# Kernel optimization log

Measured on AMD Instinct MI355X. Metric: run time of the kernel, lower is better.

The kernel has to match this reference:

```python
import jax, jax.numpy as jnp
import numpy as np

N_NODES = 50000
N_EDGES = 600000
IN_CH = 128
HID = 128
OUT_CH = 16
N_REL = 8
NEG_SLOPE = 0.2


def glorot(key, shape):
    fan_in, fan_out = shape[-2], shape[-1]
    lim = (6.0 / (fan_in + fan_out)) ** 0.5
    return jax.random.uniform(key, shape, jnp.float32, -lim, lim)


def setup_inputs() -> dict:
    key = jax.random.key(0)
    ks = jax.random.split(key, 16)
    x = jax.random.normal(ks[0], (N_NODES, IN_CH), jnp.float32)
    edge_index = jax.random.randint(ks[1], (2, N_EDGES), 0, N_NODES, jnp.int64)
    edge_type = jax.random.randint(ks[2], (N_EDGES,), 0, N_REL, jnp.int64)
    return {
        "x": x,
        "W1": glorot(ks[3], (N_REL, IN_CH, HID)),
        "q1": glorot(ks[4], (HID, 1)),
        "k1": glorot(ks[5], (HID, 1)),
        "b1": jnp.zeros((HID,), jnp.float32),
        "W2": glorot(ks[6], (N_REL, HID, HID)),
        "q2": glorot(ks[7], (HID, 1)),
        "k2": glorot(ks[8], (HID, 1)),
        "b2": jnp.zeros((HID,), jnp.float32),
        "lin_w": glorot(ks[9], (HID, OUT_CH)),
        "lin_b": jnp.zeros((OUT_CH,), jnp.float32),
        "edge_index": edge_index,
        "edge_type": edge_type,
    }


def rgat_conv(x, W, q, k, b, src, dst, etype, n_nodes):
    # Per-relation linear transform of all nodes: [R, N, H]
    xw = jnp.einsum('ni,rio->rno', x, W)
    hj = xw[etype, src]  # transformed source features per edge [E, H]
    hi = xw[etype, dst]  # transformed target features per edge [E, H]
    # additive self-attention logits (heads=1, dim=1): [E, 1]
    a = jax.nn.leaky_relu(hi @ q + hj @ k, NEG_SLOPE)
    # segment softmax over incoming edges of each target node (across-relation)
    amax = jax.ops.segment_max(a, dst, num_segments=n_nodes)  # [N, 1]
    e = jnp.exp(a - amax[dst])
    denom = jax.ops.segment_sum(e, dst, num_segments=n_nodes)  # [N, 1]
    alpha = e / denom[dst]
    # weighted scatter-add aggregation + bias
    out = jax.ops.segment_sum(alpha * hj, dst, num_segments=n_nodes)
    return out + b


def reference(x, W1, q1, k1, b1, W2, q2, k2, b2, lin_w, lin_b, edge_index, edge_type):
    src, dst = edge_index[0], edge_index[1]
    n = x.shape[0]
    h = jax.nn.relu(rgat_conv(x, W1, q1, k1, b1, src, dst, edge_type, n))
    h = jax.nn.relu(rgat_conv(h, W2, q2, k2, b2, src, dst, edge_type, n))
    h = h @ lin_w + lin_b                 # [N, out]
    g = jnp.mean(h, axis=0, keepdims=True)  # global_mean_pool -> [1, out]
    return jax.nn.log_softmax(g, axis=-1)
```

## Files before the change

### kernel.cpp

```cpp
#include <hip/hip_runtime.h>

#define CH 128
#define N_REL 8
#define OUT_CH 16
#define NEG_SLOPE 0.2f

typedef short short8 __attribute__((ext_vector_type(8)));
typedef float f32x4 __attribute__((ext_vector_type(4)));

__device__ __forceinline__ unsigned short f2bf(float f) {
    unsigned u = __float_as_uint(f);
    return (unsigned short)((u + 0x7fffu + ((u >> 16) & 1u)) >> 16);
}


__device__ __forceinline__ void dev_cast(const float* __restrict__ X,
                                         unsigned short* __restrict__ Xb,
                                         long total, int b, int tid) {
    long i = ((long)b * 256 + tid) * 8;
    if (i >= total) return;
    float4 v0 = *(const float4*)(X + i);
    float4 v1 = *(const float4*)(X + i + 4);
    ushort4 a, c;
    a.x = f2bf(v0.x); a.y = f2bf(v0.y); a.z = f2bf(v0.z); a.w = f2bf(v0.w);
    c.x = f2bf(v1.x); c.y = f2bf(v1.y); c.z = f2bf(v1.z); c.w = f2bf(v1.w);
    *(ushort4*)(Xb + i) = a;
    *(ushort4*)(Xb + i + 4) = c;
}

__device__ __forceinline__ void dev_wqk(const float* __restrict__ W,
                                        const float* __restrict__ qv,
                                        const float* __restrict__ kv,
                                        float* __restrict__ wq, float* __restrict__ wk,
                                        int rb, int tid) {
    int r = rb * 2 + (tid >> 7);
    int i = tid & 127;
    const float* row = W + ((size_t)r * CH + i) * CH;
    float aq = 0.f, ak = 0.f;
    for (int o = 0; o < CH; ++o) { float w = row[o]; aq += w * qv[o]; ak += w * kv[o]; }
    wq[r * CH + i] = aq;
    wk[r * CH + i] = ak;
}

__device__ __forceinline__ void dev_wpack(const float* __restrict__ W,
                                          unsigned short* __restrict__ Wpk, int t) {
    int lane = t & 63, ks = (t >> 6) & 3, ct = (t >> 8) & 7, r = t >> 11;
    int l15 = lane & 15, g = lane >> 4;
    const float* src = W + ((size_t)r * CH + ks * 32 + g * 8) * CH + ct * 16 + l15;
    unsigned pk[4];
    #pragma unroll
    for (int p = 0; p < 4; ++p) {
        unsigned lo = f2bf(src[(2 * p) * CH]);
        unsigned hi = f2bf(src[(2 * p + 1) * CH]);
        pk[p] = lo | (hi << 16);
    }
    *(uint4*)(Wpk + (size_t)t * 8) = make_uint4(pk[0], pk[1], pk[2], pk[3]);
}

__device__ __forceinline__ void dev_qkpack(const float* __restrict__ wq,
                                           const float* __restrict__ wk,
                                           unsigned short* __restrict__ qkf, int tid) {
    int lane = tid & 63, ks = tid >> 6;
    int j = lane & 15, g = lane >> 4;
    const float* col = (j < 8) ? (wq + j * CH) : (wk + (j - 8) * CH);
    int k0 = ks * 32 + g * 8;
    unsigned pk[4];
    #pragma unroll
    for (int p = 0; p < 4; ++p) {
        unsigned lo = f2bf(col[k0 + 2 * p]);
        unsigned hi = f2bf(col[k0 + 2 * p + 1]);
        pk[p] = lo | (hi << 16);
    }
    *(uint4*)(qkf + (size_t)tid * 8) = make_uint4(pk[0], pk[1], pk[2], pk[3]);
}


__global__ void k_cast_hist(const float* __restrict__ X, unsigned short* __restrict__ Xb,
                            long total, const int* __restrict__ dst,
                            int* __restrict__ count, int ne, int nb_cast) {
    int b = blockIdx.x, tid = threadIdx.x;
    if (b < nb_cast) {
        dev_cast(X, Xb, total, b, tid);
    } else {
        int e = (b - nb_cast) * 256 + tid;
        if (e < ne) atomicAdd(count + dst[e], 1);
    }
}

__global__ __launch_bounds__(256) void k_scan1_wqk(const int* __restrict__ count,
                                                   int* __restrict__ rowptr,
                                                   int* __restrict__ bsum, int n, int nbscan,
                                                   const float* __restrict__ W,
                                                   const float* __restrict__ qv,
                                                   const float* __restrict__ kv,
                                                   float* __restrict__ wq,
                                                   float* __restrict__ wk) {
    int b = blockIdx.x, tid = threadIdx.x;
    if (b >= nbscan) { dev_wqk(W, qv, kv, wq, wk, b - nbscan, tid); return; }
    __shared__ int wsum[4];
    int lane = tid & 63, w = tid >> 6;
    int i0 = b * 1024 + tid * 4;
    int v0 = 0, v1 = 0, v2 = 0, v3 = 0;
    if (i0 + 3 < n) {
        int4 v = *(const int4*)(count + i0);
        v0 = v.x; v1 = v.y; v2 = v.z; v3 = v.w;
    } else {
        if (i0 < n) v0 = count[i0];
        if (i0 + 1 < n) v1 = count[i0 + 1];
        if (i0 + 2 < n) v2 = count[i0 + 2];
        if (i0 + 3 < n) v3 = count[i0 + 3];
    }
    int t1 = v0 + v1, t2 = t1 + v2, t3 = t2 + v3;
    int s = t3;
    #pragma unroll
    for (int off = 1; off < 64; off <<= 1) {
        int t = __shfl_up(s, off);
        if (lane >= off) s += t;
    }
    if (lane == 63) wsum[w] = s;
    __syncthreads();
    int wpre = 0;
    #pragma unroll
    for (int i = 0; i < 4; ++i) wpre += (i < w) ? wsum[i] : 0;
    int excl = wpre + s - t3;
    if (i0 < n) rowptr[i0] = excl;
    if (i0 + 1 < n) rowptr[i0 + 1] = excl + v0;
    if (i0 + 2 < n) rowptr[i0 + 2] = excl + t1;
    if (i0 + 3 < n) rowptr[i0 + 3] = excl + t2;
    if (tid == 0) bsum[b] = wsum[0] + wsum[1] + wsum[2] + wsum[3];
}

__global__ __launch_bounds__(256) void k_scan2_wprep(int* __restrict__ bsum,
                                                     int* __restrict__ total, int nb,
                                                     const float* __restrict__ W,
                                                     unsigned short* __restrict__ Wpk,
                                                     const float* __restrict__ wq,
                                                     const float* __restrict__ wk,
                                                     unsigned short* __restrict__ qkf) {
    int b = blockIdx.x, tid = threadIdx.x;
    if (b == 0) {
        if (tid >= 64) return;
        int lane = tid;
        int carry = 0;
        for (int base = 0; base < nb; base += 64) {
            int i = base + lane;
            int v = (i < nb) ? bsum[i] : 0;
            int s = v;
            #pragma unroll
            for (int off = 1; off < 64; off <<= 1) {
                int t = __shfl_up(s, off);
                if (lane >= off) s += t;
            }
            if (i < nb) bsum[i] = carry + s - v;
            carry += __shfl(s, 63);
        }
        if (lane == 0) *total = carry;
    } else if (b <= 64) {
        dev_wpack(W, Wpk, (b - 1) * 256 + tid);
    } else {
        dev_qkpack(wq, wk, qkf, tid);
    }
}

__global__ __launch_bounds__(256) void k_scan3(int* __restrict__ rowptr,
                                               int* __restrict__ rowptr_work,
                                               const int* __restrict__ bsum,
                                               const int* __restrict__ total, int n) {
    int b = blockIdx.x;
    int i0 = b * 1024 + threadIdx.x * 4;
    int add = bsum[b];
    #pragma unroll
    for (int j = 0; j < 4; ++j) {
        int i = i0 + j;
        if (i < n) {
            int v = rowptr[i] + add;
            rowptr[i] = v;
            rowptr_work[i] = v;
        }
    }
    if (b == 0 && threadIdx.x == 0) rowptr[n] = *total;
}


__global__ __launch_bounds__(256) void k_fat(
    const unsigned short* __restrict__ Xb, const unsigned short* __restrict__ Wpk,
    const unsigned short* __restrict__ qkf, unsigned short* __restrict__ XW,
    float* __restrict__ sq, float* __restrict__ sk, int n,
    int nb_gemm, int nb_sqsk,
    const int* __restrict__ esrc, const int* __restrict__ edst,
    const int* __restrict__ etp, int* __restrict__ rowptr_work,
    int* __restrict__ pe, int ne) {
    __shared__ unsigned short lds_w[32 * 64 * 8];
    const int b = blockIdx.x, tid = threadIdx.x;
    const int wv = tid >> 6, lane = tid & 63;
    const int l15 = lane & 15, g = lane >> 4;
    const int ntiles = (n + 15) >> 4;

    if (b < nb_gemm) {
        const int r = b & 7;
        const int nslots = (nb_gemm >> 3) * 4;
        const int slot0 = (b >> 3) * 4 + wv;

        const unsigned short* wsrc = Wpk + (size_t)r * 32 * 64 * 8;
        #pragma unroll
        for (int i = 0; i < 8; ++i) {
            int idx = tid + i * 256;
            *(uint4*)(lds_w + idx * 8) = *(const uint4*)(wsrc + (size_t)idx * 8);
        }
        __syncthreads();

        for (int t = slot0; t < ntiles; t += nslots) {
            int row = t * 16 + l15;
            bool ok = row < n;
            int rowc = ok ? row : n - 1;
            const unsigned short* xrow = Xb + (size_t)rowc * CH + g * 8;
            short8 xf[4];
            #pragma unroll
            for (int ks = 0; ks < 4; ++ks) xf[ks] = *(const short8*)(xrow + ks * 32);
            unsigned short* orow = XW + ((size_t)r * n + row) * CH;
            #pragma unroll
            for (int ct = 0; ct < 8; ++ct) {
                f32x4 a = {0.f, 0.f, 0.f, 0.f};
                #pragma unroll
                for (int ks = 0; ks < 4; ++ks) {
                    short8 wf = *(const short8*)(lds_w + ((ct * 4 + ks) * 64 + lane) * 8);
                    a = __builtin_amdgcn_mfma_f32_16x16x32_bf16(wf, xf[ks], a, 0, 0, 0);
                }
                unsigned p01, p23;
                asm("v_cvt_pk_bf16_f32 %0, %1, %2" : "=v"(p01) : "v"(a[0]), "v"(a[1]));
                asm("v_cvt_pk_bf16_f32 %0, %1, %2" : "=v"(p23) : "v"(a[2]), "v"(a[3]));
                if (ok) *(uint2*)(orow + ct * 16 + g * 4) = make_uint2(p01, p23);
            }
        }
    } else if (b < nb_gemm + nb_sqsk) {
        const int t = (b - nb_gemm) * 4 + wv;
        if (t >= ntiles) return;
        short8 qf[4];
        #pragma unroll
        for (int ks = 0; ks < 4; ++ks)
            qf[ks] = *(const short8*)(qkf + (size_t)(ks * 64 + lane) * 8);
        int row = t * 16 + l15;
        bool ok = row < n;
        int rowc = ok ? row : n - 1;
        const unsigned short* xrow = Xb + (size_t)rowc * CH + g * 8;
        short8 xf[4];
        #pragma unroll
        for (int ks = 0; ks < 4; ++ks) xf[ks] = *(const short8*)(xrow + ks * 32);
        f32x4 dq = {0.f, 0.f, 0.f, 0.f};
        #pragma unroll
        for (int ks = 0; ks < 4; ++ks)
            dq = __builtin_amdgcn_mfma_f32_16x16x32_bf16(qf[ks], xf[ks], dq, 0, 0, 0);
        if (ok) {
            float* base = (g < 2) ? sq : sk;
            int j0 = (g & 1) * 4;
            #pragma unroll
            for (int reg = 0; reg < 4; ++reg)
                base[(size_t)(j0 + reg) * n + row] = dq[reg];
        }
    } else {
        int e = (b - nb_gemm - nb_sqsk) * 256 + tid;
        if (e >= ne) return;
        int pos = atomicAdd(rowptr_work + edst[e], 1);
        pe[pos] = (esrc[e] & 0xffff) | (etp[e] << 16);
    }
}


__global__ __launch_bounds__(256) void k_attn_wqk(
    const int* __restrict__ rowptr, const int* __restrict__ pe,
    const float* __restrict__ sq, const float* __restrict__ sk,
    const unsigned short* __restrict__ XW, const float* __restrict__ bias,
    unsigned short* __restrict__ outb, int n_nodes,
    const float* __restrict__ Wn, const float* __restrict__ qn,
    const float* __restrict__ kn, float* __restrict__ wqn,
    float* __restrict__ wkn, int nb_wqk) {
    int b = blockIdx.x;
    if (b < nb_wqk) { dev_wqk(Wn, qn, kn, wqn, wkn, b, threadIdx.x); return; }
    int wid = ((b - nb_wqk) * 256 + threadIdx.x) >> 6;
    int lane = threadIdx.x & 63;
    if (wid >= n_nodes) return;
    const int l16 = lane & 15, g16 = lane >> 4;
    int r0 = rowptr[wid], r1 = rowptr[wid + 1];
    float acc[8] = {};
    float denom = 0.f;

    if (r1 > r0) {
        float sqv = (lane < N_REL) ? sq[lane * n_nodes + wid] : 0.f;

        float m = -1e30f;
        for (int c0 = r0; c0 < r1; c0 += 64) {
            int j = c0 + lane;
            float a = -1e30f;
            if (j < r1) {
                int p = pe[j];
                int s = p & 0xffff, t = p >> 16;
                float av = __shfl(sqv, t) + sk[t * n_nodes + s];
                a = av >= 0.f ? av : NEG_SLOPE * av;
            }
            m = fmaxf(m, a);
        }
        #pragma unroll
        for (int off = 32; off; off >>= 1) m = fmaxf(m, __shfl_xor(m, off));

        for (int c0 = r0; c0 < r1; c0 += 64) {
            int j = c0 + lane;
            float ev = 0.f;
            int p = 0;
            if (j < r1) {
                p = pe[j];
                int s = p & 0xffff, t = p >> 16;
                float av = __shfl(sqv, t) + sk[t * n_nodes + s];
                av = av >= 0.f ? av : NEG_SLOPE * av;
                ev = __expf(av - m);
            }
            float evs = ev;
            #pragma unroll
            for (int off = 32; off; off >>= 1) evs += __shfl_xor(evs, off);
            denom += evs;

            int C = r1 - c0;
            if (C > 64) C = 64;
            for (int jj = 0; jj < C; jj += 4) {
                int lsel = jj + g16;
                float evj = __shfl(ev, lsel);
                int pj = __shfl(p, lsel);
                int s = pj & 0xffff, t = pj >> 16;
                const unsigned short* row = XW + ((size_t)(t * n_nodes + s)) * CH + l16 * 8;
                uint4 v = *(const uint4*)row;
                acc[0] += evj * __uint_as_float(v.x << 16);
                acc[1] += evj * __uint_as_float(v.x & 0xffff0000u);
                acc[2] += evj * __uint_as_float(v.y << 16);
                acc[3] += evj * __uint_as_float(v.y & 0xffff0000u);
                acc[4] += evj * __uint_as_float(v.z << 16);
                acc[5] += evj * __uint_as_float(v.z & 0xffff0000u);
                acc[6] += evj * __uint_as_float(v.w << 16);
                acc[7] += evj * __uint_as_float(v.w & 0xffff0000u);
            }
        }
    }

    #pragma unroll
    for (int i = 0; i < 8; ++i) {
        acc[i] += __shfl_xor(acc[i], 16);
        acc[i] += __shfl_xor(acc[i], 32);
    }

    if (lane < 16) {
        float inv = denom > 0.f ? 1.f / denom : 0.f;
        unsigned pk[4];
        #pragma unroll
        for (int i = 0; i < 4; ++i) {
            float b0 = bias[l16 * 8 + 2 * i];
            float b1 = bias[l16 * 8 + 2 * i + 1];
            float o0 = acc[2 * i] * inv + b0;
            float o1 = acc[2 * i + 1] * inv + b1;
            o0 = o0 > 0.f ? o0 : 0.f;
            o1 = o1 > 0.f ? o1 : 0.f;
            pk[i] = (unsigned)f2bf(o0) | ((unsigned)f2bf(o1) << 16);
        }
        *(uint4*)(outb + (size_t)wid * CH + l16 * 8) = make_uint4(pk[0], pk[1], pk[2], pk[3]);
    }
}


__global__ __launch_bounds__(256) void k_wprep2(const float* __restrict__ W,
                                                unsigned short* __restrict__ Wpk,
                                                const float* __restrict__ wq,
                                                const float* __restrict__ wk,
                                                unsigned short* __restrict__ qkf) {
    int b = blockIdx.x, tid = threadIdx.x;
    if (b < 64) dev_wpack(W, Wpk, b * 256 + tid);
    else dev_qkpack(wq, wk, qkf, tid);
}


__global__ __launch_bounds__(256) void k_colsum(const unsigned short* __restrict__ h,
                                                float* __restrict__ sum, int n_nodes) {
    __shared__ float cs[CH];
    int tid = threadIdx.x;
    int c2 = (tid & 63) * 2;
    int rw = tid >> 6;
    if (tid < CH) cs[tid] = 0.f;
    __syncthreads();
    float a0 = 0.f, a1 = 0.f;
    for (int row = blockIdx.x * 4 + rw; row < n_nodes; row += gridDim.x * 4) {
        unsigned v = *(const unsigned*)(h + (size_t)row * CH + c2);
        a0 += __uint_as_float(v << 16);
        a1 += __uint_as_float(v & 0xffff0000u);
    }
    atomicAdd(&cs[c2], a0);
    atomicAdd(&cs[c2 + 1], a1);
    __syncthreads();
    if (tid < CH) atomicAdd(sum + tid, cs[tid]);
}

__global__ void k_head(const float* __restrict__ sum, const float* __restrict__ lw,
                       const float* __restrict__ lb, float* __restrict__ outp, int n_nodes) {
    __shared__ float mean[CH];
    int t = threadIdx.x;
    mean[t] = sum[t] / (float)n_nodes;
    __syncthreads();
    if (t < OUT_CH) {
        float g = lb[t];
        for (int i = 0; i < CH; ++i) g += mean[i] * lw[i * OUT_CH + t];
        float m = g;
        #pragma unroll
        for (int off = 8; off; off >>= 1) m = fmaxf(m, __shfl_xor(m, off, 16));
        float ex = expf(g - m);
        float se = ex;
        #pragma unroll
        for (int off = 8; off; off >>= 1) se += __shfl_xor(se, off, 16);
        outp[t] = g - m - logf(se);
    }
}

extern "C" void kernel_launch(void* const* d_in, const int* in_sizes, int n_in,
                              void* d_out, int out_size, void* d_ws, size_t ws_size,
                              hipStream_t stream) {
    const float* x  = (const float*)d_in[0];
    const float* W1 = (const float*)d_in[1];
    const float* q1 = (const float*)d_in[2];
    const float* k1 = (const float*)d_in[3];
    const float* b1 = (const float*)d_in[4];
    const float* W2 = (const float*)d_in[5];
    const float* q2 = (const float*)d_in[6];
    const float* k2 = (const float*)d_in[7];
    const float* b2 = (const float*)d_in[8];
    const float* lw = (const float*)d_in[9];
    const float* lb = (const float*)d_in[10];
    const int* ei   = (const int*)d_in[11];
    const int* etp  = (const int*)d_in[12];

    const int n  = in_sizes[0] / CH;
    const int ne = in_sizes[12];
    const int* esrc = ei;
    const int* edst = ei + ne;

    char* ws = (char*)d_ws;
    size_t off = 0;
    auto carve = [&](size_t bytes) -> char* {
        char* p = ws + off;
        off = (off + bytes + 255) & ~(size_t)255;
        return p;
    };
    unsigned short* xw  = (unsigned short*)carve((size_t)N_REL * n * CH * 2);
    unsigned short* xb  = (unsigned short*)carve((size_t)n * CH * 2);
    unsigned short* h1b = (unsigned short*)carve((size_t)n * CH * 2);
    unsigned short* h2b = (unsigned short*)carve((size_t)n * CH * 2);
    unsigned short* wpk = (unsigned short*)carve((size_t)N_REL * 32 * 64 * 8 * 2);
    unsigned short* qkf = (unsigned short*)carve((size_t)256 * 8 * 2);
    float* sq     = (float*)carve((size_t)N_REL * n * 4);
    float* sk     = (float*)carve((size_t)N_REL * n * 4);
    float* wq     = (float*)carve(N_REL * CH * 4);
    float* wk     = (float*)carve(N_REL * CH * 4);
    int* count    = (int*)carve((size_t)n * 4);
    int* rowptr   = (int*)carve((size_t)(n + 1) * 4);
    int* rowptr_w = (int*)carve((size_t)n * 4);
    int* pe       = (int*)carve((size_t)ne * 4);
    int* bsum     = (int*)carve((size_t)256 * 4);
    int* total    = (int*)carve(4);
    float* sum128 = (float*)carve(CH * 4);

    hipMemsetAsync(count, 0, (size_t)n * 4, stream);
    hipMemsetAsync(sum128, 0, CH * 4, stream);

    const int nbscan = (n + 1023) / 1024;
    const int nb_cast = (int)(((long)n * CH / 8 + 255) / 256);
    const int nb_hist = (ne + 255) / 256;
    const int nb_gemm = 512;
    const int ntiles = (n + 15) >> 4;
    const int nb_sqsk = (ntiles + 3) / 4;
    const int nb_scat = (ne + 255) / 256;
    const int nb_attn = (n + 3) / 4;

    k_cast_hist<<<nb_cast + nb_hist, 256, 0, stream>>>(x, xb, (long)n * CH, edst, count, ne, nb_cast);
    k_scan1_wqk<<<nbscan + 4, 256, 0, stream>>>(count, rowptr, bsum, n, nbscan, W1, q1, k1, wq, wk);
    k_scan2_wprep<<<66, 256, 0, stream>>>(bsum, total, nbscan, W1, wpk, wq, wk, qkf);
    k_scan3<<<nbscan, 256, 0, stream>>>(rowptr, rowptr_w, bsum, total, n);
    k_fat<<<nb_gemm + nb_sqsk + nb_scat, 256, 0, stream>>>(xb, wpk, qkf, xw, sq, sk, n,
                                                           nb_gemm, nb_sqsk,
                                                           esrc, edst, etp, rowptr_w, pe, ne);
    k_attn_wqk<<<4 + nb_attn, 256, 0, stream>>>(rowptr, pe, sq, sk, xw, b1, h1b, n,
                                                W2, q2, k2, wq, wk, 4);
    k_wprep2<<<65, 256, 0, stream>>>(W2, wpk, wq, wk, qkf);
    k_fat<<<nb_gemm + nb_sqsk, 256, 0, stream>>>(h1b, wpk, qkf, xw, sq, sk, n,
                                                 nb_gemm, nb_sqsk,
                                                 esrc, edst, etp, rowptr_w, pe, 0);
    k_attn_wqk<<<nb_attn, 256, 0, stream>>>(rowptr, pe, sq, sk, xw, b2, h2b, n,
                                            (const float*)nullptr, (const float*)nullptr,
                                            (const float*)nullptr, (float*)nullptr,
                                            (float*)nullptr, 0);

    k_colsum<<<256, 256, 0, stream>>>(h2b, sum128, n);
    k_head<<<1, CH, 0, stream>>>(sum128, lw, lb, (float*)d_out, n);
}
```

Before: 247.2 us.

## Keep per-wave weight fragments in registers and split column tiles across waves

After: 290.1 us. 1.17x slower.

```diff
diff --git a/kernel.cpp b/kernel.cpp
--- a/kernel.cpp
+++ b/kernel.cpp
@@ -190,7 +190,6 @@
     const int* __restrict__ esrc, const int* __restrict__ edst,
     const int* __restrict__ etp, int* __restrict__ rowptr_work,
     int* __restrict__ pe, int ne) {
-    __shared__ unsigned short lds_w[32 * 64 * 8];
     const int b = blockIdx.x, tid = threadIdx.x;
     const int wv = tid >> 6, lane = tid & 63;
     const int l15 = lane & 15, g = lane >> 4;
@@ -198,18 +197,19 @@
 
     if (b < nb_gemm) {
         const int r = b & 7;
-        const int nslots = (nb_gemm >> 3) * 4;
-        const int slot0 = (b >> 3) * 4 + wv;
-
-        const unsigned short* wsrc = Wpk + (size_t)r * 32 * 64 * 8;
-        #pragma unroll
-        for (int i = 0; i < 8; ++i) {
-            int idx = tid + i * 256;
-            *(uint4*)(lds_w + idx * 8) = *(const uint4*)(wsrc + (size_t)idx * 8);
-        }
-        __syncthreads();
-
-        for (int t = slot0; t < ntiles; t += nslots) {
+        const int bslot = b >> 3;
+        const int nbslots = nb_gemm >> 3;
+        const int ctA = wv, ctB = wv + 4;
+
+        short8 wfA[4], wfB[4];
+        const unsigned short* wr = Wpk + (size_t)r * 32 * 64 * 8 + (size_t)lane * 8;
+        #pragma unroll
+        for (int ks = 0; ks < 4; ++ks) {
+            wfA[ks] = *(const short8*)(wr + (size_t)(ctA * 4 + ks) * 64 * 8);
+            wfB[ks] = *(const short8*)(wr + (size_t)(ctB * 4 + ks) * 64 * 8);
+        }
+
+        for (int t = bslot; t < ntiles; t += nbslots) {
             int row = t * 16 + l15;
             bool ok = row < n;
             int rowc = ok ? row : n - 1;
@@ -217,19 +217,23 @@
             short8 xf[4];
             #pragma unroll
             for (int ks = 0; ks < 4; ++ks) xf[ks] = *(const short8*)(xrow + ks * 32);
-            unsigned short* orow = XW + ((size_t)r * n + row) * CH;
+
+            f32x4 a = {0.f, 0.f, 0.f, 0.f};
+            f32x4 c = {0.f, 0.f, 0.f, 0.f};
             #pragma unroll
-            for (int ct = 0; ct < 8; ++ct) {
-                f32x4 a = {0.f, 0.f, 0.f, 0.f};
-                #pragma unroll
-                for (int ks = 0; ks < 4; ++ks) {
-                    short8 wf = *(const short8*)(lds_w + ((ct * 4 + ks) * 64 + lane) * 8);
-                    a = __builtin_amdgcn_mfma_f32_16x16x32_bf16(wf, xf[ks], a, 0, 0, 0);
-                }
-                unsigned p01, p23;
-                asm("v_cvt_pk_bf16_f32 %0, %1, %2" : "=v"(p01) : "v"(a[0]), "v"(a[1]));
-                asm("v_cvt_pk_bf16_f32 %0, %1, %2" : "=v"(p23) : "v"(a[2]), "v"(a[3]));
-                if (ok) *(uint2*)(orow + ct * 16 + g * 4) = make_uint2(p01, p23);
+            for (int ks = 0; ks < 4; ++ks) {
+                a = __builtin_amdgcn_mfma_f32_16x16x32_bf16(wfA[ks], xf[ks], a, 0, 0, 0);
+                c = __builtin_amdgcn_mfma_f32_16x16x32_bf16(wfB[ks], xf[ks], c, 0, 0, 0);
+            }
+            unsigned a01, a23, c01, c23;
+            asm("v_cvt_pk_bf16_f32 %0, %1, %2" : "=v"(a01) : "v"(a[0]), "v"(a[1]));
+            asm("v_cvt_pk_bf16_f32 %0, %1, %2" : "=v"(a23) : "v"(a[2]), "v"(a[3]));
+            asm("v_cvt_pk_bf16_f32 %0, %1, %2" : "=v"(c01) : "v"(c[0]), "v"(c[1]));
+            asm("v_cvt_pk_bf16_f32 %0, %1, %2" : "=v"(c23) : "v"(c[2]), "v"(c[3]));
+            if (ok) {
+                unsigned short* orow = XW + ((size_t)r * n + row) * CH;
+                *(uint2*)(orow + ctA * 16 + g * 4) = make_uint2(a01, a23);
+                *(uint2*)(orow + ctB * 16 + g * 4) = make_uint2(c01, c23);
             }
         }
     } else if (b < nb_gemm + nb_sqsk) {
```
